# Kernel tuning notes

Measured on AMD Instinct MI355X. Metric: run time of the kernel, lower is better.

The kernel has to match this reference:

```python
import jax, jax.numpy as jnp
import numpy as np

DIM = 256
NUM_HEADS = 4
HEAD_DIM = DIM // NUM_HEADS
SCALE = HEAD_DIM ** -0.5


def setup_inputs() -> dict:
    key = jax.random.key(0)
    ks = jax.random.split(key, 9)
    B, P, C = 4, 4096, DIM
    s = 0.02
    return {
        "x": jax.random.normal(ks[0], (B, P, C), dtype=jnp.float32),
        "Wq": jax.random.normal(ks[1], (C, C), dtype=jnp.float32) * s,
        "bq": jnp.zeros((C,), dtype=jnp.float32),
        "Wk": jax.random.normal(ks[2], (C, C), dtype=jnp.float32) * s,
        "bk": jnp.zeros((C,), dtype=jnp.float32),
        "Wv": jax.random.normal(ks[3], (C, C), dtype=jnp.float32) * s,
        "bv": jnp.zeros((C,), dtype=jnp.float32),
        "Wo": jax.random.normal(ks[4], (C, C), dtype=jnp.float32) * s,
        "bo": jnp.zeros((C,), dtype=jnp.float32),
    }


def reference(x, Wq, bq, Wk, bk, Wv, bv, Wo, bo):
    B, P, C = x.shape
    H, D = NUM_HEADS, C // NUM_HEADS
    q = (x @ Wq + bq).reshape(B, P, H, D)
    k = (x @ Wk + bk).reshape(B, P, H, D)
    v = (x @ Wv + bv).reshape(B, P, H, D)
    # att[b,p,q,h] = sum_d q[b,p,h,d]*scale * k[b,q,h,d]
    att = jnp.einsum('bphd,bqhd->bpqh', q * SCALE, k)
    att = jax.nn.softmax(att, axis=2)
    out = jnp.einsum('bpqh,bqhd->bphd', att, v).reshape(B, P, C)
    return out @ Wo + bo
```

## Files before the change

### kernel.cpp

```cpp
#include <hip/hip_runtime.h>
#include <hip/hip_bf16.h>

#define DIMC 256
#define NHEADS 4
#define HDIM 64
#define BATCH 4
#define SEQ 4096
#define MTOT (BATCH*SEQ)
#define SCALE_LOG2E 0.18033688011112042f

typedef __attribute__((ext_vector_type(8))) __bf16 bf16x8;
typedef __attribute__((ext_vector_type(4))) __bf16 bf16x4;
typedef __attribute__((ext_vector_type(2))) __bf16 bf16x2;
typedef __attribute__((ext_vector_type(4))) float f32x4;
typedef __attribute__((ext_vector_type(2))) unsigned uint2v;
typedef __attribute__((ext_vector_type(4))) unsigned uint4v;

__device__ inline void gll16(const void* g, void* l) {
  __builtin_amdgcn_global_load_lds((const __attribute__((address_space(1))) unsigned int*)g,
                                   (__attribute__((address_space(3))) unsigned int*)l, 16, 0, 0);
}

__device__ inline float vexp2(float x) { return __builtin_amdgcn_exp2f(x); }

__device__ inline unsigned pack2(float lo, float hi) {
  bf16x2 p; p[0] = (__bf16)lo; p[1] = (__bf16)hi;
  return __builtin_bit_cast(unsigned, p);
}

__device__ inline bf16x8 swzread(const __bf16* base, int row, int c16) {
  return *reinterpret_cast<const bf16x8*>(
      reinterpret_cast<const char*>(base) + row * 128 + ((c16 ^ (row & 7)) << 4));
}


__global__ __launch_bounds__(256) void cvt_x_kernel(const float* __restrict__ x, __bf16* __restrict__ xb) {
  int i = (blockIdx.x * 256 + threadIdx.x) * 4;
  float4 v = *reinterpret_cast<const float4*>(x + i);
  bf16x4 o;
  o[0] = (__bf16)v.x; o[1] = (__bf16)v.y; o[2] = (__bf16)v.z; o[3] = (__bf16)v.w;
  *reinterpret_cast<bf16x4*>(xb + i) = o;
}

__global__ __launch_bounds__(256) void prep_w(const float* __restrict__ Wq, const float* __restrict__ Wk,
                                              const float* __restrict__ Wv, const float* __restrict__ Wo,
                                              __bf16* __restrict__ wqkvt, __bf16* __restrict__ wot) {
  int row = blockIdx.x;
  int k = threadIdx.x;
  if (row < 768) {
    const float* src; float scale = 1.f; int n = row & 255;
    if (row < 256)      { src = Wq; scale = SCALE_LOG2E; }
    else if (row < 512) { src = Wk; }
    else                { src = Wv; }
    wqkvt[row * 256 + k] = (__bf16)(src[k * 256 + n] * scale);
  } else {
    int n = row - 768;
    wot[n * 256 + k] = (__bf16)(Wo[k * 256 + n]);
  }
}

__global__ __launch_bounds__(256) void prep_bias(const float* __restrict__ bq, const float* __restrict__ bk,
                                                 const float* __restrict__ bv, float* __restrict__ biasq) {
  int i = blockIdx.x * 256 + threadIdx.x;
  biasq[i] = (i < 256) ? bq[i] * SCALE_LOG2E : (i < 512 ? bk[i - 256] : bv[i - 512]);
}

template<int MODE>
__global__ __launch_bounds__(256) void gemm_bt(const __bf16* __restrict__ A, const __bf16* __restrict__ Bt,
                                               const float* __restrict__ bias,
                                               __bf16* __restrict__ q_ws, __bf16* __restrict__ k_ws,
                                               __bf16* __restrict__ v_ws, float* __restrict__ fout) {
  __shared__ __align__(16) __bf16 As[128 * 64];
  __shared__ __align__(16) __bf16 Bs[128 * 64];
  const int tid = threadIdx.x;
  const int lane = tid & 63, wave = tid >> 6;
  const int wr = wave >> 1, wc = wave & 1;
  const int r16 = lane & 15, g4 = lane >> 4;
  const int m0 = blockIdx.y * 128, n0 = blockIdx.x * 128;
  f32x4 acc[4][4] = {};
  for (int k0 = 0; k0 < DIMC; k0 += 64) {
    #pragma unroll
    for (int it = 0; it < 4; ++it) {
      int e = it * 256 + tid;
      int r = e >> 3, c = e & 7;
      int cs = c ^ (r & 7);
      gll16(A  + (size_t)(m0 + r) * DIMC + k0 + cs * 8, As + e * 8);
      gll16(Bt + (size_t)(n0 + r) * DIMC + k0 + cs * 8, Bs + e * 8);
    }
    __syncthreads();
    #pragma unroll
    for (int kk = 0; kk < 2; ++kk) {
      bf16x8 af[4], bfr[4];
      #pragma unroll
      for (int mi = 0; mi < 4; ++mi)
        af[mi] = swzread(As, wr * 64 + mi * 16 + r16, kk * 4 + g4);
      #pragma unroll
      for (int ni = 0; ni < 4; ++ni)
        bfr[ni] = swzread(Bs, wc * 64 + ni * 16 + r16, kk * 4 + g4);
      #pragma unroll
      for (int mi = 0; mi < 4; ++mi)
        #pragma unroll
        for (int ni = 0; ni < 4; ++ni)
          acc[mi][ni] = __builtin_amdgcn_mfma_f32_16x16x32_bf16(af[mi], bfr[ni], acc[mi][ni], 0, 0, 0);
    }
    __syncthreads();
  }
  #pragma unroll
  for (int mi = 0; mi < 4; ++mi)
    #pragma unroll
    for (int ni = 0; ni < 4; ++ni)
      #pragma unroll
      for (int r = 0; r < 4; ++r) {
        int m = m0 + wr * 64 + mi * 16 + g4 * 4 + r;
        int n = n0 + wc * 64 + ni * 16 + r16;
        float v = acc[mi][ni][r] + bias[n];
        if (MODE == 0) {
          int b = m >> 12, p = m & 4095;
          int sect = n >> 8, nc = n & 255;
          int h = nc >> 6, d = nc & 63;
          __bf16 hv = (__bf16)v;
          size_t off = ((size_t)(b * NHEADS + h) * SEQ + p) * HDIM + d;
          if (sect == 0)      q_ws[off] = hv;
          else if (sect == 1) k_ws[off] = hv;
          else                v_ws[off] = hv;
        } else {
          fout[(size_t)m * DIMC + n] = v;
        }
      }
}

__global__ __launch_bounds__(256) void transpose_v(const __bf16* __restrict__ v_ws, __bf16* __restrict__ vt_ws) {
  __shared__ __align__(16) __bf16 t[64][72];
  int bh = blockIdx.y, p0 = blockIdx.x * 64;
  int tid = threadIdx.x;
  const __bf16* src = v_ws + ((size_t)bh * SEQ + p0) * HDIM;
  #pragma unroll
  for (int it = 0; it < 2; ++it) {
    int e = it * 256 + tid;
    int pr = e >> 3, c = (e & 7) * 8;
    bf16x8 val = *reinterpret_cast<const bf16x8*>(src + pr * HDIM + c);
    #pragma unroll
    for (int j = 0; j < 8; ++j) t[c + j][pr] = val[j];
  }
  __syncthreads();
  __bf16* dst = vt_ws + (size_t)bh * HDIM * SEQ + p0;
  #pragma unroll
  for (int it = 0; it < 2; ++it) {
    int e = it * 256 + tid;
    int d = e >> 3, c = (e & 7) * 8;
    bf16x8 val = *reinterpret_cast<const bf16x8*>(&t[d][c]);
    *reinterpret_cast<bf16x8*>(dst + (size_t)d * SEQ + c) = val;
  }
}

__global__ __launch_bounds__(256, 4) void attn_kernel(const __bf16* __restrict__ q_ws, const __bf16* __restrict__ k_ws,
                                                      const __bf16* __restrict__ vt_ws,
                                                      float* __restrict__ o_num, float* __restrict__ lsum) {
  __shared__ __align__(16) __bf16 Ks[2][64 * 64];
  __shared__ __align__(16) __bf16 Vts[2][64 * 64];
  const int tid = threadIdx.x;
  const int lane = tid & 63;
  const int r16 = lane & 15, g4 = lane >> 4;
  int bid = blockIdx.x;
  int wg = (bid & 7) * 128 + (bid >> 3);
  int bh = wg >> 6, rrw = wg & 63;
  int qb = rrw >> 1, half = rrw & 1;
  int b = bh >> 2, h = bh & 3;
  const __bf16* Qp  = q_ws  + (size_t)bh * SEQ * HDIM;
  const __bf16* Kp  = k_ws  + (size_t)bh * SEQ * HDIM;
  const __bf16* Vtp = vt_ws + (size_t)bh * HDIM * SEQ;
  const int q0 = qb * 128 + (tid >> 6) * 32;
  const int kvb = half * (SEQ / 2);
  bf16x8 qf[2][2];
  #pragma unroll
  for (int hh = 0; hh < 2; ++hh)
    #pragma unroll
    for (int kk = 0; kk < 2; ++kk)
      qf[hh][kk] = *reinterpret_cast<const bf16x8*>(Qp + (size_t)(q0 + hh * 16 + r16) * HDIM + kk * 32 + g4 * 8);
  f32x4 o_acc[2][4] = {};
  f32x4 rsv[2] = {};

  const int sr = tid >> 3;
  const int scs = (tid & 7) ^ (sr & 7);
  const __bf16* kSrc = Kp  + (size_t)sr * HDIM + scs * 8;
  const __bf16* vSrc = Vtp + (size_t)sr * SEQ  + scs * 8;

  #define STAGE(buf, kv0) do { \
      gll16(kSrc + (size_t)(kv0) * HDIM,        &Ks[buf][tid * 8]); \
      gll16(kSrc + (size_t)((kv0) + 32) * HDIM, &Ks[buf][(tid + 256) * 8]); \
      gll16(vSrc + (kv0),                       &Vts[buf][tid * 8]); \
      gll16(vSrc + 32 * SEQ + (kv0),            &Vts[buf][(tid + 256) * 8]); \
    } while (0)

  STAGE(0, kvb);
  __syncthreads();

  int cur = 0;
  for (int t = 0; t < SEQ / 128; ++t) {
    if (t + 1 < SEQ / 128) STAGE(cur ^ 1, kvb + (t + 1) * 64);
    f32x4 s0[4] = {}, s1[4] = {};
    #pragma unroll
    for (int ni = 0; ni < 4; ++ni)
      #pragma unroll
      for (int kk = 0; kk < 2; ++kk) {
        bf16x8 kf = swzread(Ks[cur], ni * 16 + r16, kk * 4 + g4);
        s0[ni] = __builtin_amdgcn_mfma_f32_16x16x32_bf16(kf, qf[0][kk], s0[ni], 0, 0, 0);
        s1[ni] = __builtin_amdgcn_mfma_f32_16x16x32_bf16(kf, qf[1][kk], s1[ni], 0, 0, 0);
      }
    bf16x8 pa[2][2];
    #pragma unroll
    for (int hh = 0; hh < 2; ++hh) {
      unsigned c[4][2];
      #pragma unroll
      for (int ni = 0; ni < 4; ++ni) {
        const f32x4& sv = hh ? s1[ni] : s0[ni];
        float p0 = vexp2(sv[0]), p1 = vexp2(sv[1]);
        float p2 = vexp2(sv[2]), p3 = vexp2(sv[3]);
        rsv[hh] += (f32x4){p0, p1, p2, p3};
        c[ni][0] = pack2(p0, p1);
        c[ni][1] = pack2(p2, p3);
      }
      unsigned tt[2][4];
      #pragma unroll
      for (int kk = 0; kk < 2; ++kk)
        #pragma unroll
        for (int u = 0; u < 2; ++u) {
          uint2v p = __builtin_amdgcn_permlane32_swap(c[2 * kk][u], c[2 * kk + 1][u], false, false);
          uint2v q = __builtin_amdgcn_permlane16_swap(p[0], p[1], false, false);
          tt[kk][u]     = q[0];
          tt[kk][2 + u] = q[1];
        }
      uint4v w0 = {tt[0][0], tt[0][1], tt[0][2], tt[0][3]};
      uint4v w1 = {tt[1][0], tt[1][1], tt[1][2], tt[1][3]};
      pa[hh][0] = __builtin_bit_cast(bf16x8, w0);
      pa[hh][1] = __builtin_bit_cast(bf16x8, w1);
    }
    #pragma unroll
    for (int kk = 0; kk < 2; ++kk)
      #pragma unroll
      for (int di = 0; di < 4; ++di) {
        bf16x8 vf = swzread(Vts[cur], di * 16 + r16, kk * 4 + g4);
        o_acc[0][di] = __builtin_amdgcn_mfma_f32_16x16x32_bf16(pa[0][kk], vf, o_acc[0][di], 0, 0, 0);
        o_acc[1][di] = __builtin_amdgcn_mfma_f32_16x16x32_bf16(pa[1][kk], vf, o_acc[1][di], 0, 0, 0);
      }
    __syncthreads();
    cur ^= 1;
  }
  #pragma unroll
  for (int hh = 0; hh < 2; ++hh) {
    float den = (rsv[hh][0] + rsv[hh][1]) + (rsv[hh][2] + rsv[hh][3]);
    den += __shfl_xor(den, 16);
    den += __shfl_xor(den, 32);
    if (lane < 16) atomicAdd(&lsum[(size_t)bh * SEQ + q0 + hh * 16 + r16], den);
  }
  #pragma unroll
  for (int hh = 0; hh < 2; ++hh)
    #pragma unroll
    for (int di = 0; di < 4; ++di)
      #pragma unroll
      for (int r = 0; r < 4; ++r) {
        int q = q0 + hh * 16 + g4 * 4 + r;
        atomicAdd(&o_num[(size_t)(b * SEQ + q) * DIMC + h * HDIM + di * 16 + r16], o_acc[hh][di][r]);
      }
}

__global__ __launch_bounds__(256) void normalize_o(const float* __restrict__ on, const float* __restrict__ lsum,
                                                   __bf16* __restrict__ o_ws) {
  int i = blockIdx.x * 256 + threadIdx.x;
  int flat = i * 4;
  int m = flat >> 8, c = flat & 255;
  int h = c >> 6;
  int b = m >> 12, p = m & 4095;
  float inv = 1.f / lsum[(size_t)(b * NHEADS + h) * SEQ + p];
  float4 n = *reinterpret_cast<const float4*>(on + flat);
  bf16x4 o;
  o[0] = (__bf16)(n.x * inv); o[1] = (__bf16)(n.y * inv);
  o[2] = (__bf16)(n.z * inv); o[3] = (__bf16)(n.w * inv);
  *reinterpret_cast<bf16x4*>(o_ws + flat) = o;
}


extern "C" void kernel_launch(void* const* d_in, const int* in_sizes, int n_in,
                              void* d_out, int out_size, void* d_ws, size_t ws_size,
                              hipStream_t stream) {
  const float* x  = (const float*)d_in[0];
  const float* Wq = (const float*)d_in[1];
  const float* bq = (const float*)d_in[2];
  const float* Wk = (const float*)d_in[3];
  const float* bk = (const float*)d_in[4];
  const float* Wv = (const float*)d_in[5];
  const float* bv = (const float*)d_in[6];
  const float* Wo = (const float*)d_in[7];
  const float* bo = (const float*)d_in[8];
  float* out = (float*)d_out;

  const size_t NE = (size_t)MTOT * DIMC;
  char* w = (char*)d_ws;
  __bf16* q_ws  = (__bf16*)w; w += NE * 2;
  __bf16* k_ws  = (__bf16*)w; w += NE * 2;
  __bf16* vt_ws = (__bf16*)w; w += NE * 2;
  __bf16* wqkvt = (__bf16*)w; w += (size_t)768 * 256 * 2;
  __bf16* wot   = (__bf16*)w; w += (size_t)256 * 256 * 2;
  float*  biasq = (float*)w;  w += 768 * 4;
  float*  lsum  = (float*)w;  w += (size_t)16 * SEQ * 4;
  float*  o_num = (float*)w;  w += NE * 4;
  __bf16* xb   = (__bf16*)o_num;
  __bf16* v_ws = (__bf16*)((char*)o_num + NE * 2);
  __bf16* o_ws = q_ws;

  cvt_x_kernel<<<MTOT * DIMC / 1024, 256, 0, stream>>>(x, xb);
  prep_w<<<1024, 256, 0, stream>>>(Wq, Wk, Wv, Wo, wqkvt, wot);
  prep_bias<<<3, 256, 0, stream>>>(bq, bk, bv, biasq);
  gemm_bt<0><<<dim3(6, 128), 256, 0, stream>>>(xb, wqkvt, biasq, q_ws, k_ws, v_ws, nullptr);
  transpose_v<<<dim3(64, 16), 256, 0, stream>>>(v_ws, vt_ws);
  hipMemsetAsync(lsum, 0, (size_t)16 * SEQ * 4 + NE * 4, stream);
  attn_kernel<<<1024, 256, 0, stream>>>(q_ws, k_ws, vt_ws, o_num, lsum);
  normalize_o<<<NE / 1024, 256, 0, stream>>>(o_num, lsum, o_ws);
  gemm_bt<1><<<dim3(2, 128), 256, 0, stream>>>(o_ws, wot, bo, nullptr, nullptr, nullptr, out);
}
```

Before: 144.8 us.

## Fold V transpose into QKV GEMM epilogue, merge bias prep, prioritize MFMA waves

The QKV projection GEMM now writes V directly in transposed (d-major) layout, which removes the separate transpose_v kernel and its staging buffer. The bias prep is merged into prep_w as three extra blocks, saving a kernel launch. The attention loop wraps its MFMA sections in s_setprio to favour matrix issue over the exp/permute phase of other waves. The transposed V stores from the epilogue are strided by SEQ and may coalesce poorly.

```diff
diff --git a/kernel.cpp b/kernel.cpp
--- a/kernel.cpp
+++ b/kernel.cpp
@@ -44,7 +44,10 @@
 
 __global__ __launch_bounds__(256) void prep_w(const float* __restrict__ Wq, const float* __restrict__ Wk,
                                               const float* __restrict__ Wv, const float* __restrict__ Wo,
-                                              __bf16* __restrict__ wqkvt, __bf16* __restrict__ wot) {
+                                              const float* __restrict__ bq, const float* __restrict__ bk,
+                                              const float* __restrict__ bv,
+                                              __bf16* __restrict__ wqkvt, __bf16* __restrict__ wot,
+                                              float* __restrict__ biasq) {
   int row = blockIdx.x;
   int k = threadIdx.x;
   if (row < 768) {
@@ -53,23 +56,20 @@
     else if (row < 512) { src = Wk; }
     else                { src = Wv; }
     wqkvt[row * 256 + k] = (__bf16)(src[k * 256 + n] * scale);
-  } else {
+  } else if (row < 1024) {
     int n = row - 768;
     wot[n * 256 + k] = (__bf16)(Wo[k * 256 + n]);
-  }
-}
-
-__global__ __launch_bounds__(256) void prep_bias(const float* __restrict__ bq, const float* __restrict__ bk,
-                                                 const float* __restrict__ bv, float* __restrict__ biasq) {
-  int i = blockIdx.x * 256 + threadIdx.x;
-  biasq[i] = (i < 256) ? bq[i] * SCALE_LOG2E : (i < 512 ? bk[i - 256] : bv[i - 512]);
+  } else {
+    int i = (row - 1024) * 256 + k;
+    biasq[i] = (i < 256) ? bq[i] * SCALE_LOG2E : (i < 512 ? bk[i - 256] : bv[i - 512]);
+  }
 }
 
 template<int MODE>
 __global__ __launch_bounds__(256) void gemm_bt(const __bf16* __restrict__ A, const __bf16* __restrict__ Bt,
                                                const float* __restrict__ bias,
                                                __bf16* __restrict__ q_ws, __bf16* __restrict__ k_ws,
-                                               __bf16* __restrict__ v_ws, float* __restrict__ fout) {
+                                               __bf16* __restrict__ vt_ws, float* __restrict__ fout) {
   __shared__ __align__(16) __bf16 As[128 * 64];
   __shared__ __align__(16) __bf16 Bs[128 * 64];
   const int tid = threadIdx.x;
@@ -119,38 +119,14 @@
           int sect = n >> 8, nc = n & 255;
           int h = nc >> 6, d = nc & 63;
           __bf16 hv = (__bf16)v;
-          size_t off = ((size_t)(b * NHEADS + h) * SEQ + p) * HDIM + d;
-          if (sect == 0)      q_ws[off] = hv;
-          else if (sect == 1) k_ws[off] = hv;
-          else                v_ws[off] = hv;
+          size_t bhb = (size_t)(b * NHEADS + h);
+          if (sect == 0)      q_ws[(bhb * SEQ + p) * HDIM + d] = hv;
+          else if (sect == 1) k_ws[(bhb * SEQ + p) * HDIM + d] = hv;
+          else                vt_ws[(bhb * HDIM + d) * SEQ + p] = hv;
         } else {
           fout[(size_t)m * DIMC + n] = v;
         }
       }
-}
-
-__global__ __launch_bounds__(256) void transpose_v(const __bf16* __restrict__ v_ws, __bf16* __restrict__ vt_ws) {
-  __shared__ __align__(16) __bf16 t[64][72];
-  int bh = blockIdx.y, p0 = blockIdx.x * 64;
-  int tid = threadIdx.x;
-  const __bf16* src = v_ws + ((size_t)bh * SEQ + p0) * HDIM;
-  #pragma unroll
-  for (int it = 0; it < 2; ++it) {
-    int e = it * 256 + tid;
-    int pr = e >> 3, c = (e & 7) * 8;
-    bf16x8 val = *reinterpret_cast<const bf16x8*>(src + pr * HDIM + c);
-    #pragma unroll
-    for (int j = 0; j < 8; ++j) t[c + j][pr] = val[j];
-  }
-  __syncthreads();
-  __bf16* dst = vt_ws + (size_t)bh * HDIM * SEQ + p0;
-  #pragma unroll
-  for (int it = 0; it < 2; ++it) {
-    int e = it * 256 + tid;
-    int d = e >> 3, c = (e & 7) * 8;
-    bf16x8 val = *reinterpret_cast<const bf16x8*>(&t[d][c]);
-    *reinterpret_cast<bf16x8*>(dst + (size_t)d * SEQ + c) = val;
-  }
 }
 
 __global__ __launch_bounds__(256, 4) void attn_kernel(const __bf16* __restrict__ q_ws, const __bf16* __restrict__ k_ws,
@@ -199,6 +175,7 @@
   for (int t = 0; t < SEQ / 128; ++t) {
     if (t + 1 < SEQ / 128) STAGE(cur ^ 1, kvb + (t + 1) * 64);
     f32x4 s0[4] = {}, s1[4] = {};
+    __builtin_amdgcn_s_setprio(1);
     #pragma unroll
     for (int ni = 0; ni < 4; ++ni)
       #pragma unroll
@@ -207,6 +184,7 @@
         s0[ni] = __builtin_amdgcn_mfma_f32_16x16x32_bf16(kf, qf[0][kk], s0[ni], 0, 0, 0);
         s1[ni] = __builtin_amdgcn_mfma_f32_16x16x32_bf16(kf, qf[1][kk], s1[ni], 0, 0, 0);
       }
+    __builtin_amdgcn_s_setprio(0);
     bf16x8 pa[2][2];
     #pragma unroll
     for (int hh = 0; hh < 2; ++hh) {
@@ -235,6 +213,7 @@
       pa[hh][0] = __builtin_bit_cast(bf16x8, w0);
       pa[hh][1] = __builtin_bit_cast(bf16x8, w1);
     }
+    __builtin_amdgcn_s_setprio(1);
     #pragma unroll
     for (int kk = 0; kk < 2; ++kk)
       #pragma unroll
@@ -243,6 +222,7 @@
         o_acc[0][di] = __builtin_amdgcn_mfma_f32_16x16x32_bf16(pa[0][kk], vf, o_acc[0][di], 0, 0, 0);
         o_acc[1][di] = __builtin_amdgcn_mfma_f32_16x16x32_bf16(pa[1][kk], vf, o_acc[1][di], 0, 0, 0);
       }
+    __builtin_amdgcn_s_setprio(0);
     __syncthreads();
     cur ^= 1;
   }
@@ -305,14 +285,11 @@
   float*  lsum  = (float*)w;  w += (size_t)16 * SEQ * 4;
   float*  o_num = (float*)w;  w += NE * 4;
   __bf16* xb   = (__bf16*)o_num;
-  __bf16* v_ws = (__bf16*)((char*)o_num + NE * 2);
   __bf16* o_ws = q_ws;
 
   cvt_x_kernel<<<MTOT * DIMC / 1024, 256, 0, stream>>>(x, xb);
-  prep_w<<<1024, 256, 0, stream>>>(Wq, Wk, Wv, Wo, wqkvt, wot);
-  prep_bias<<<3, 256, 0, stream>>>(bq, bk, bv, biasq);
-  gemm_bt<0><<<dim3(6, 128), 256, 0, stream>>>(xb, wqkvt, biasq, q_ws, k_ws, v_ws, nullptr);
-  transpose_v<<<dim3(64, 16), 256, 0, stream>>>(v_ws, vt_ws);
+  prep_w<<<1027, 256, 0, stream>>>(Wq, Wk, Wv, Wo, bq, bk, bv, wqkvt, wot, biasq);
+  gemm_bt<0><<<dim3(6, 128), 256, 0, stream>>>(xb, wqkvt, biasq, q_ws, k_ws, vt_ws, nullptr);
   hipMemsetAsync(lsum, 0, (size_t)16 * SEQ * 4 + NE * 4, stream);
   attn_kernel<<<1024, 256, 0, stream>>>(q_ws, k_ws, vt_ws, o_num, lsum);
   normalize_o<<<NE / 1024, 256, 0, stream>>>(o_num, lsum, o_ws);
```

New measurement: 138.3 us. -4.5%, faster.
